# Kernel optimization log

Hardware: AMD Instinct MI355X
Metric: run time of the kernel (lower is better)

Reference implementation:

```python
import jax, jax.numpy as jnp
import numpy as np

E, K, D, H, C = 32768, 32, 128, 4, 10
DH = D // H

def setup_inputs() -> dict:
    key = jax.random.key(0)
    ks = jax.random.split(key, 9)
    s = 1.0 / np.sqrt(D)
    return {
        "edge_feats": jax.random.normal(ks[0], (E, D), jnp.float32),
        "Wq": jax.random.normal(ks[1], (D, D), jnp.float32) * s,
        "Wk": jax.random.normal(ks[2], (D, D), jnp.float32) * s,
        "Wv": jax.random.normal(ks[3], (D, D), jnp.float32) * s,
        "Wo": jax.random.normal(ks[4], (D, D), jnp.float32) * s,
        "W1": jax.random.normal(ks[5], (D, D), jnp.float32) * s,
        "b1": jnp.zeros((D,), jnp.float32),
        "W2": jax.random.normal(ks[6], (D, C), jnp.float32) * s,
        "b2": jnp.zeros((C,), jnp.float32),
        "edge_adj": jax.random.randint(ks[7], (E, K), 0, E, jnp.int32),
    }

def reference(edge_feats, Wq, Wk, Wv, Wo, W1, b1, W2, b2, edge_adj):
    # Edge attention: each edge attends over its K adjacent edges.
    q = (edge_feats @ Wq).reshape(E, H, DH)                 # [E,H,dh]
    k_all = edge_feats @ Wk                                  # [E,D]
    v_all = edge_feats @ Wv                                  # [E,D]
    kn = k_all[edge_adj].reshape(E, K, H, DH)                # gather [E,K,H,dh]
    vn = v_all[edge_adj].reshape(E, K, H, DH)                # gather [E,K,H,dh]
    scores = jnp.einsum("ehd,ekhd->ehk", q, kn) / np.sqrt(DH)
    attn = jax.nn.softmax(scores, axis=-1)                   # [E,H,K]
    ctx = jnp.einsum("ehk,ekhd->ehd", attn, vn).reshape(E, D)
    edge_out = ctx @ Wo                                       # [E,D]
    # classifier: Linear -> GELU -> Linear
    h = jax.nn.gelu(edge_out @ W1 + b1)
    logits = h @ W2 + b2                                      # [E,C]
    return logits
```

## Files before the change

### kernel.cpp

```cpp
#include <hip/hip_runtime.h>
#include <hip/hip_bf16.h>

constexpr int E_EDGES = 32768;
constexpr int DIM = 128;

using bf16x8 = __attribute__((ext_vector_type(8))) short;
using f32x4  = __attribute__((ext_vector_type(4))) float;
typedef unsigned int uint4v __attribute__((ext_vector_type(4)));
typedef unsigned int uint2v __attribute__((ext_vector_type(2)));

__device__ inline float bflo(unsigned u) { return __uint_as_float(u << 16); }
__device__ inline float bfhi(unsigned u) { return __uint_as_float(u & 0xffff0000u); }
__device__ inline unsigned pk_bf2(float a, float b) {
    __hip_bfloat162 h = __float22bfloat162_rn(make_float2(a, b));
    return *(unsigned*)&h;
}

__global__ __launch_bounds__(256) void k_prep(
    const float* __restrict__ Wq, const float* __restrict__ Wk,
    const float* __restrict__ Wv, const float* __restrict__ Wo,
    const float* __restrict__ W1, __hip_bfloat16* __restrict__ Wt,
    __hip_bfloat16* __restrict__ wft) {
    const int b = blockIdx.x;
    const int t = threadIdx.x;
    if (b < 3) {
        const float* W = (b == 0) ? Wq : (b == 1) ? Wk : Wv;
        __hip_bfloat16* dst = Wt + b * 16384;
#pragma unroll
        for (int i = 0; i < 8; ++i) {
            int idx = i * 2048 + t * 8;
            int k = idx >> 7, n0 = idx & 127;
            float4 f0 = *(const float4*)(W + k * 128 + n0);
            float4 f1 = *(const float4*)(W + k * 128 + n0 + 4);
            float f[8] = {f0.x, f0.y, f0.z, f0.w, f1.x, f1.y, f1.z, f1.w};
#pragma unroll
            for (int j = 0; j < 8; ++j)
                dst[(n0 + j) * 128 + k] = __float2bfloat16(f[j]);
        }
    } else {
        int idx = (b - 3) * 256 + t;
        int r = idx >> 7, c = idx & 127;
        float acc = 0.f;
#pragma unroll 16
        for (int k = 0; k < 128; ++k)
            acc = fmaf(Wo[r * 128 + k], W1[k * 128 + c], acc);
        wft[c * 128 + r] = __float2bfloat16(acc);
    }
}

__global__ __launch_bounds__(256) void k_qkv(
    const float* __restrict__ feats, const __hip_bfloat16* __restrict__ Wt,
    __hip_bfloat16* __restrict__ qp, __hip_bfloat16* __restrict__ kp,
    __hip_bfloat16* __restrict__ vp) {
    __shared__ short Als[16384];
    __shared__ short Bls[16384];

    const int t = threadIdx.x;
    const int lane = t & 63;
    const int w = t >> 6;
    const int wm = w >> 1, wn = w & 1;
    const int row0 = blockIdx.x * 128;

#pragma unroll
    for (int i = 0; i < 8; ++i) {
        int idx = i * 2048 + t * 8;
        int r = idx >> 7, k0 = idx & 127;
        float4 f0 = *(const float4*)(feats + (size_t)(row0 + r) * DIM + k0);
        float4 f1 = *(const float4*)(feats + (size_t)(row0 + r) * DIM + k0 + 4);
        uint4 o = make_uint4(pk_bf2(f0.x, f0.y), pk_bf2(f0.z, f0.w),
                             pk_bf2(f1.x, f1.y), pk_bf2(f1.z, f1.w));
        *(uint4*)&Als[(r * 128 + k0) ^ ((r & 7) << 3)] = o;
    }
#pragma unroll
    for (int i = 0; i < 8; ++i) {
        int idx = i * 2048 + t * 8;
        int n = idx >> 7, k0 = idx & 127;
        uint4 v = *(const uint4*)(Wt + n * 128 + k0);
        *(uint4*)&Bls[(n * 128 + k0) ^ ((n & 7) << 3)] = v;
    }
    __syncthreads();

    bf16x8 afr[4][4];
#pragma unroll
    for (int m = 0; m < 4; ++m)
#pragma unroll
        for (int ks = 0; ks < 4; ++ks) {
            int r = wm * 64 + m * 16 + (lane & 15);
            int kb = ks * 32 + (lane >> 4) * 8;
            afr[m][ks] = *(bf16x8*)&Als[(r * 128 + kb) ^ ((r & 7) << 3)];
        }

    for (int proj = 0; proj < 3; ++proj) {
        f32x4 acc[4][4];
#pragma unroll
        for (int m = 0; m < 4; ++m)
#pragma unroll
            for (int n = 0; n < 4; ++n) acc[m][n] = (f32x4){0.f, 0.f, 0.f, 0.f};

#pragma unroll
        for (int ks = 0; ks < 4; ++ks) {
            bf16x8 bfr[4];
#pragma unroll
            for (int n = 0; n < 4; ++n) {
                int nn = wn * 64 + n * 16 + (lane & 15);
                int kb = ks * 32 + (lane >> 4) * 8;
                bfr[n] = *(bf16x8*)&Bls[(nn * 128 + kb) ^ ((nn & 7) << 3)];
            }
#pragma unroll
            for (int m = 0; m < 4; ++m)
#pragma unroll
                for (int n = 0; n < 4; ++n)
                    acc[m][n] = __builtin_amdgcn_mfma_f32_16x16x32_bf16(
                        afr[m][ks], bfr[n], acc[m][n], 0, 0, 0);
        }

        {
            __hip_bfloat16* dst = (proj == 0) ? qp : (proj == 1) ? kp : vp;
#pragma unroll
            for (int n = 0; n < 4; ++n) {
                int c = wn * 64 + n * 16 + (lane & 15);
                int h = c >> 5, pr = h & 1;
                int slot = ((h >> 1) << 5) + (c & 31);
                size_t base = (size_t)pr * E_EDGES * 64 + slot;
#pragma unroll
                for (int m = 0; m < 4; ++m) {
                    int rb = row0 + wm * 64 + m * 16 + (lane >> 4) * 4;
#pragma unroll
                    for (int r = 0; r < 4; ++r)
                        dst[base + (size_t)(rb + r) * 64] =
                            __float2bfloat16(acc[m][n][r]);
                }
            }
        }

        if (proj < 2) {
            __syncthreads();
#pragma unroll
            for (int i = 0; i < 8; ++i) {
                int idx = i * 2048 + t * 8;
                int n = idx >> 7, k0 = idx & 127;
                uint4 v = *(const uint4*)(Wt + (proj + 1) * 16384 + n * 128 + k0);
                *(uint4*)&Bls[(n * 128 + k0) ^ ((n & 7) << 3)] = v;
            }
            __syncthreads();
        }
    }
}

__global__ __launch_bounds__(256) void k_score(
    const __hip_bfloat16* __restrict__ qp, const __hip_bfloat16* __restrict__ kp,
    const int* __restrict__ adj, unsigned short* __restrict__ aw, int pass) {
    __shared__ int adj_s[4][32];

    const int lane = threadIdx.x & 63;
    const int wid = threadIdx.x >> 6;
    const int e = blockIdx.x * 4 + wid;
    const int n = lane & 31;
    const int g = lane >> 5;

    if (lane < 32)
        adj_s[wid][lane] = __builtin_nontemporal_load(adj + e * 32 + lane);

    const uint4v* qr =
        (const uint4v*)(qp + ((size_t)pass * E_EDGES + e) * 64 + g * 32);
    float qa[32];
#pragma unroll
    for (int j = 0; j < 4; ++j) {
        uint4v u = __builtin_nontemporal_load(qr + j);
        qa[j * 8 + 0] = bflo(u[0]); qa[j * 8 + 1] = bfhi(u[0]);
        qa[j * 8 + 2] = bflo(u[1]); qa[j * 8 + 3] = bfhi(u[1]);
        qa[j * 8 + 4] = bflo(u[2]); qa[j * 8 + 5] = bfhi(u[2]);
        qa[j * 8 + 6] = bflo(u[3]); qa[j * 8 + 7] = bfhi(u[3]);
    }

    const int row = adj_s[wid][n];
    const uint4* kr =
        (const uint4*)(kp + ((size_t)pass * E_EDGES + row) * 64 + g * 32);
    float s0 = 0.f;
#pragma unroll
    for (int j = 0; j < 4; ++j) {
        uint4 u = kr[j];
        s0 = fmaf(qa[j * 8 + 0], bflo(u.x), s0); s0 = fmaf(qa[j * 8 + 1], bfhi(u.x), s0);
        s0 = fmaf(qa[j * 8 + 2], bflo(u.y), s0); s0 = fmaf(qa[j * 8 + 3], bfhi(u.y), s0);
        s0 = fmaf(qa[j * 8 + 4], bflo(u.z), s0); s0 = fmaf(qa[j * 8 + 5], bfhi(u.z), s0);
        s0 = fmaf(qa[j * 8 + 6], bflo(u.w), s0); s0 = fmaf(qa[j * 8 + 7], bfhi(u.w), s0);
    }
    s0 *= 0.17677669529663689f;

    float m0 = s0;
#pragma unroll
    for (int off = 16; off; off >>= 1) m0 = fmaxf(m0, __shfl_xor(m0, off));
    float e0 = __expf(s0 - m0);
    float sum0 = e0;
#pragma unroll
    for (int off = 16; off; off >>= 1) sum0 += __shfl_xor(sum0, off);
    float wgt = e0 / sum0;

    __builtin_nontemporal_store(
        __bfloat16_as_ushort(__float2bfloat16(wgt)),
        aw + ((size_t)pass * E_EDGES + e) * 64 + g * 32 + n);
}

__global__ __launch_bounds__(256) void k_pv(
    const __hip_bfloat16* __restrict__ vp, const unsigned short* __restrict__ aw,
    const int* __restrict__ adj, __hip_bfloat16* __restrict__ ctxb, int pass) {
    __shared__ unsigned short aws[4][64];
    __shared__ int adj_s[4][32];

    const int lane = threadIdx.x & 63;
    const int wid = threadIdx.x >> 6;
    const int e = blockIdx.x * 4 + wid;

    if (lane < 32)
        adj_s[wid][lane] = __builtin_nontemporal_load(adj + e * 32 + lane);
    if (lane < 16) {
        uint2v a2 = __builtin_nontemporal_load(
            (const uint2v*)(aw + ((size_t)pass * E_EDGES + e) * 64) + lane);
        *(uint2v*)&aws[wid][lane * 4] = a2;
    }

    const int d4 = lane & 15;
    const int grp = lane >> 4;
    const int gi = d4 >> 3;
    float4 c = make_float4(0.f, 0.f, 0.f, 0.f);
#pragma unroll
    for (int i = 0; i < 8; ++i) {
        int nn = grp * 8 + i;
        int r2 = adj_s[wid][nn];
        float a = __uint_as_float((unsigned)aws[wid][gi * 32 + nn] << 16);
        uint2 u = *(const uint2*)(vp + ((size_t)pass * E_EDGES + r2) * 64 + d4 * 4);
        c.x = fmaf(a, bflo(u.x), c.x); c.y = fmaf(a, bfhi(u.x), c.y);
        c.z = fmaf(a, bflo(u.y), c.z); c.w = fmaf(a, bfhi(u.y), c.w);
    }
    c.x += __shfl_xor(c.x, 16); c.y += __shfl_xor(c.y, 16);
    c.z += __shfl_xor(c.z, 16); c.w += __shfl_xor(c.w, 16);
    c.x += __shfl_xor(c.x, 32); c.y += __shfl_xor(c.y, 32);
    c.z += __shfl_xor(c.z, 32); c.w += __shfl_xor(c.w, 32);
    if (lane < 16) {
        int h2 = pass + 2 * gi;
        uint2v o;
        o[0] = pk_bf2(c.x, c.y);
        o[1] = pk_bf2(c.z, c.w);
        __builtin_nontemporal_store(
            o, (uint2v*)(ctxb + (size_t)e * DIM + h2 * 32 + (d4 & 7) * 4));
    }
}

__global__ __launch_bounds__(256) void k_mlp(
    const __hip_bfloat16* __restrict__ ctxb, const __hip_bfloat16* __restrict__ wft,
    const float* __restrict__ b1, const float* __restrict__ W2,
    const float* __restrict__ b2, float* __restrict__ out) {
    __shared__ short Als[16384];
    __shared__ short Bls[16384];
    __shared__ float w2s[1280];
    __shared__ float b1s[128];
    __shared__ float b2s[16];

    const int t = threadIdx.x;
    const int lane = t & 63;
    const int w = t >> 6;
    const int wm = w >> 1, wn = w & 1;
    const int row0 = blockIdx.x * 128;

#pragma unroll
    for (int i = 0; i < 8; ++i) {
        int idx = i * 2048 + t * 8;
        int r = idx >> 7, k0 = idx & 127;
        uint4 v = *(const uint4*)(ctxb + (size_t)(row0 + r) * DIM + k0);
        *(uint4*)&Als[(r * 128 + k0) ^ ((r & 7) << 3)] = v;
    }
#pragma unroll
    for (int i = 0; i < 8; ++i) {
        int idx = i * 2048 + t * 8;
        int n = idx >> 7, k0 = idx & 127;
        uint4 v = *(const uint4*)(wft + n * 128 + k0);
        *(uint4*)&Bls[(n * 128 + k0) ^ ((n & 7) << 3)] = v;
    }
    for (int i = t; i < 1280; i += 256) w2s[i] = W2[i];
    if (t < 128) b1s[t] = b1[t];
    if (t < 10) b2s[t] = b2[t];
    __syncthreads();

    f32x4 acc[4][4];
#pragma unroll
    for (int m = 0; m < 4; ++m)
#pragma unroll
        for (int n = 0; n < 4; ++n) acc[m][n] = (f32x4){0.f, 0.f, 0.f, 0.f};

#pragma unroll
    for (int ks = 0; ks < 4; ++ks) {
        bf16x8 afr[4], bfr[4];
#pragma unroll
        for (int m = 0; m < 4; ++m) {
            int r = wm * 64 + m * 16 + (lane & 15);
            int kb = ks * 32 + (lane >> 4) * 8;
            afr[m] = *(bf16x8*)&Als[(r * 128 + kb) ^ ((r & 7) << 3)];
        }
#pragma unroll
        for (int n = 0; n < 4; ++n) {
            int nn = wn * 64 + n * 16 + (lane & 15);
            int kb = ks * 32 + (lane >> 4) * 8;
            bfr[n] = *(bf16x8*)&Bls[(nn * 128 + kb) ^ ((nn & 7) << 3)];
        }
#pragma unroll
        for (int m = 0; m < 4; ++m)
#pragma unroll
            for (int n = 0; n < 4; ++n)
                acc[m][n] = __builtin_amdgcn_mfma_f32_16x16x32_bf16(
                    afr[m], bfr[n], acc[m][n], 0, 0, 0);
    }

    __syncthreads();
#pragma unroll
    for (int m = 0; m < 4; ++m) {
        int lr0 = wm * 64 + m * 16 + (lane >> 4) * 4;
#pragma unroll
        for (int n = 0; n < 4; ++n) {
            int c = wn * 64 + n * 16 + (lane & 15);
            float bc = b1s[c];
#pragma unroll
            for (int r = 0; r < 4; ++r) {
                float x = acc[m][n][r] + bc;
                float u = 0.7978845608028654f * (x + 0.044715f * x * x * x);
                float ex = __expf(2.f * u);
                float th = 1.f - 2.f / (ex + 1.f);
                float h = 0.5f * x * (1.f + th);
                int lr = lr0 + r;
                Als[(lr * 128 + c) ^ ((lr & 7) << 3)] =
                    (short)(__bfloat16_as_ushort(__float2bfloat16(h)));
            }
        }
    }
    __syncthreads();

    {
        int r = t >> 1;
        int c0 = (t & 1) * 5;
        float a0 = b2s[c0], a1 = b2s[c0 + 1], a2 = b2s[c0 + 2],
              a3 = b2s[c0 + 3], a4 = b2s[c0 + 4];
#pragma unroll 8
        for (int kk = 0; kk < 128; ++kk) {
            float hv = __uint_as_float(
                ((unsigned)(unsigned short)Als[(r * 128 + kk) ^ ((r & 7) << 3)]) << 16);
            const float* wrow = &w2s[kk * 10 + c0];
            a0 = fmaf(hv, wrow[0], a0);
            a1 = fmaf(hv, wrow[1], a1);
            a2 = fmaf(hv, wrow[2], a2);
            a3 = fmaf(hv, wrow[3], a3);
            a4 = fmaf(hv, wrow[4], a4);
        }
        float* o = out + (size_t)(row0 + r) * 10 + c0;
        o[0] = a0; o[1] = a1; o[2] = a2; o[3] = a3; o[4] = a4;
    }
}

extern "C" void kernel_launch(void* const* d_in, const int* in_sizes, int n_in,
                              void* d_out, int out_size, void* d_ws, size_t ws_size,
                              hipStream_t stream) {
    const float* feats = (const float*)d_in[0];
    const float* Wq    = (const float*)d_in[1];
    const float* Wk    = (const float*)d_in[2];
    const float* Wv    = (const float*)d_in[3];
    const float* Wo    = (const float*)d_in[4];
    const float* W1    = (const float*)d_in[5];
    const float* b1    = (const float*)d_in[6];
    const float* W2    = (const float*)d_in[7];
    const float* b2    = (const float*)d_in[8];
    const int*   adj   = (const int*)d_in[9];
    float* out = (float*)d_out;

    const size_t ED2 = (size_t)E_EDGES * 64;
    __hip_bfloat16* base = (__hip_bfloat16*)d_ws;
    __hip_bfloat16* qp   = base;
    __hip_bfloat16* kp   = qp + 2 * ED2;
    __hip_bfloat16* vp   = kp + 2 * ED2;
    __hip_bfloat16* ctxb = vp + 2 * ED2;
    unsigned short* aw   = (unsigned short*)(ctxb + 2 * ED2);
    __hip_bfloat16* wt   = (__hip_bfloat16*)(aw + 2 * ED2);
    __hip_bfloat16* wft  = wt + 3 * 16384;

    k_prep<<<67, 256, 0, stream>>>(Wq, Wk, Wv, Wo, W1, wt, wft);
    k_qkv<<<E_EDGES / 128, 256, 0, stream>>>(feats, wt, qp, kp, vp);
    k_score<<<E_EDGES / 4, 256, 0, stream>>>(qp, kp, adj, aw, 0);
    k_score<<<E_EDGES / 4, 256, 0, stream>>>(qp, kp, adj, aw, 1);
    k_pv<<<E_EDGES / 4, 256, 0, stream>>>(vp, aw, adj, ctxb, 0);
    k_pv<<<E_EDGES / 4, 256, 0, stream>>>(vp, aw, adj, ctxb, 1);
    k_mlp<<<E_EDGES / 128, 256, 0, stream>>>(ctxb, wft, b1, W2, b2, out);
}
```

Baseline: 119.0 us.

## Fuse score softmax and PV gather into one attention kernel

Merges the score/softmax kernel and the attention-weighted V gather kernel into a single kernel, with both head-pair passes covered by a 2D grid. Attention weights stay in shared memory as fp32 instead of being written to and re-read from a global bf16 buffer, and four launches become one. The adjacency indices are loaded once per edge instead of twice. The fused kernel may use more registers, and there is no explicit barrier between the shared-memory write and read, which relies on each wavefront reading only its own slot.

```diff
diff --git a/kernel.cpp b/kernel.cpp
--- a/kernel.cpp
+++ b/kernel.cpp
@@ -147,11 +147,14 @@
     }
 }
 
-__global__ __launch_bounds__(256) void k_score(
+__global__ __launch_bounds__(256) void k_attn(
     const __hip_bfloat16* __restrict__ qp, const __hip_bfloat16* __restrict__ kp,
-    const int* __restrict__ adj, unsigned short* __restrict__ aw, int pass) {
+    const __hip_bfloat16* __restrict__ vp, const int* __restrict__ adj,
+    __hip_bfloat16* __restrict__ ctxb) {
+    __shared__ float attn_s[4][64];
     __shared__ int adj_s[4][32];
 
+    const int pass = blockIdx.y;
     const int lane = threadIdx.x & 63;
     const int wid = threadIdx.x >> 6;
     const int e = blockIdx.x * 4 + wid;
@@ -194,30 +197,7 @@
     float sum0 = e0;
 #pragma unroll
     for (int off = 16; off; off >>= 1) sum0 += __shfl_xor(sum0, off);
-    float wgt = e0 / sum0;
-
-    __builtin_nontemporal_store(
-        __bfloat16_as_ushort(__float2bfloat16(wgt)),
-        aw + ((size_t)pass * E_EDGES + e) * 64 + g * 32 + n);
-}
-
-__global__ __launch_bounds__(256) void k_pv(
-    const __hip_bfloat16* __restrict__ vp, const unsigned short* __restrict__ aw,
-    const int* __restrict__ adj, __hip_bfloat16* __restrict__ ctxb, int pass) {
-    __shared__ unsigned short aws[4][64];
-    __shared__ int adj_s[4][32];
-
-    const int lane = threadIdx.x & 63;
-    const int wid = threadIdx.x >> 6;
-    const int e = blockIdx.x * 4 + wid;
-
-    if (lane < 32)
-        adj_s[wid][lane] = __builtin_nontemporal_load(adj + e * 32 + lane);
-    if (lane < 16) {
-        uint2v a2 = __builtin_nontemporal_load(
-            (const uint2v*)(aw + ((size_t)pass * E_EDGES + e) * 64) + lane);
-        *(uint2v*)&aws[wid][lane * 4] = a2;
-    }
+    attn_s[wid][g * 32 + n] = e0 / sum0;
 
     const int d4 = lane & 15;
     const int grp = lane >> 4;
@@ -227,7 +207,7 @@
     for (int i = 0; i < 8; ++i) {
         int nn = grp * 8 + i;
         int r2 = adj_s[wid][nn];
-        float a = __uint_as_float((unsigned)aws[wid][gi * 32 + nn] << 16);
+        float a = attn_s[wid][gi * 32 + nn];
         uint2 u = *(const uint2*)(vp + ((size_t)pass * E_EDGES + r2) * 64 + d4 * 4);
         c.x = fmaf(a, bflo(u.x), c.x); c.y = fmaf(a, bfhi(u.x), c.y);
         c.z = fmaf(a, bflo(u.y), c.z); c.w = fmaf(a, bfhi(u.y), c.w);
@@ -375,15 +355,11 @@
     __hip_bfloat16* kp   = qp + 2 * ED2;
     __hip_bfloat16* vp   = kp + 2 * ED2;
     __hip_bfloat16* ctxb = vp + 2 * ED2;
-    unsigned short* aw   = (unsigned short*)(ctxb + 2 * ED2);
-    __hip_bfloat16* wt   = (__hip_bfloat16*)(aw + 2 * ED2);
+    __hip_bfloat16* wt   = ctxb + 2 * ED2;
     __hip_bfloat16* wft  = wt + 3 * 16384;
 
     k_prep<<<67, 256, 0, stream>>>(Wq, Wk, Wv, Wo, W1, wt, wft);
     k_qkv<<<E_EDGES / 128, 256, 0, stream>>>(feats, wt, qp, kp, vp);
-    k_score<<<E_EDGES / 4, 256, 0, stream>>>(qp, kp, adj, aw, 0);
-    k_score<<<E_EDGES / 4, 256, 0, stream>>>(qp, kp, adj, aw, 1);
-    k_pv<<<E_EDGES / 4, 256, 0, stream>>>(vp, aw, adj, ctxb, 0);
-    k_pv<<<E_EDGES / 4, 256, 0, stream>>>(vp, aw, adj, ctxb, 1);
+    k_attn<<<dim3(E_EDGES / 4, 2), 256, 0, stream>>>(qp, kp, vp, adj, ctxb);
     k_mlp<<<E_EDGES / 128, 256, 0, stream>>>(ctxb, wft, b1, W2, b2, out);
 }
```

New measurement: 103.7 us. -12.9%, faster.
